# Kernel optimization log

Measured on AMD Instinct MI355X. Metric: run time of the kernel, lower is better.

The kernel has to match this reference:

```python
import jax, jax.numpy as jnp
import numpy as np

ODE_UNFOLDS = 6   # ncps LTCCell default
EPS = 1e-8
BATCH = 4096

def _conv(x, w, b, stride, pad):
    y = jax.lax.conv_general_dilated(x, w, (stride, stride), [(pad, pad), (pad, pad)],
                                     dimension_numbers=('NCHW', 'OIHW', 'NCHW'))
    return y + b[None, :, None, None]

def _bn(x, g, bta, m, v):
    # eval-mode batchnorm (running stats)
    inv = g * jax.lax.rsqrt(v + 1e-5)
    return x * inv[None, :, None, None] + (bta - m * inv)[None, :, None, None]

def _maxpool2(x):
    return jax.lax.reduce_window(x, -jnp.inf, jax.lax.max, (1, 1, 2, 2), (1, 1, 2, 2), 'VALID')

def _forward(x, conv1_w, conv1_b, conv2_w, conv2_b, bn2_g, bn2_b, bn2_m, bn2_v,
             conv3_w, conv3_b, conv4_w, conv4_b, bn4_g, bn4_b, bn4_m, bn4_v,
             input_w, input_b, sensory_mu, sensory_sigma, sensory_w, sensory_erev, sensory_mask,
             mu, sigma, w, erev, mask, gleak, vleak, cm, output_w, output_b):
    h = jax.nn.relu(_conv(x, conv1_w, conv1_b, 1, 0))                                            # [B,16,26,26]
    h = jax.nn.relu(_bn(_conv(h, conv2_w, conv2_b, 2, 2), bn2_g, bn2_b, bn2_m, bn2_v))           # [B,32,14,14]
    h = jax.nn.relu(_conv(h, conv3_w, conv3_b, 2, 2))                                            # [B,64,7,7]
    h = _maxpool2(jax.nn.relu(_bn(_conv(h, conv4_w, conv4_b, 2, 2), bn4_g, bn4_b, bn4_m, bn4_v)))  # [B,128,2,2]
    seq = h.reshape(-1, 32, 16)                                                                  # [B,T=32,F=16]
    # --- LTC cell (ncps fused ODE solver) ---
    xin = seq * input_w + input_b                                                                # affine input mapping
    # sensory synapses depend only on the input -> precompute for all timesteps
    sact = jax.nn.softplus(sensory_w) * jax.nn.sigmoid((xin[..., None] - sensory_mu) * sensory_sigma) * sensory_mask  # [B,T,16,19]
    wnum_s = jnp.einsum('btsn,sn->btn', sact, sensory_erev)   # [B,T,19]
    wden_s = jnp.sum(sact, axis=2)                            # [B,T,19]
    w_pos = jax.nn.softplus(w) * mask                         # [pre=19,post=19]
    gl = jax.nn.softplus(gleak)
    cm_t = jax.nn.softplus(cm) * ODE_UNFOLDS                  # cm / (elapsed_time=1.0 / unfolds)
    def tstep(v, nd):
        wns, wds = nd
        def unfold(v2, _):
            wa = w_pos * jax.nn.sigmoid((v2[..., None] - mu) * sigma)   # [B,19,19]
            num = cm_t * v2 + gl * vleak + jnp.sum(wa * erev, axis=1) + wns
            den = cm_t + gl + jnp.sum(wa, axis=1) + wds
            return num / (den + EPS), None
        v, _ = jax.lax.scan(unfold, v, None, length=ODE_UNFOLDS)
        return v, None
    h0 = jnp.zeros((seq.shape[0], 19), seq.dtype)
    vT, _ = jax.lax.scan(tstep, h0, (jnp.swapaxes(wnum_s, 0, 1), jnp.swapaxes(wden_s, 0, 1)))
    # out[:, -1, :] == output mapping of final state; motor neurons are the first 2
    return vT[:, :2] * output_w + output_b


def setup_inputs() -> dict:
    key = jax.random.key(0)
    ks = jax.random.split(key, 16)
    rng = np.random.default_rng(0)
    u = lambda k, s, lo, hi: jax.random.uniform(k, s, jnp.float32, lo, hi)
    n = lambda k, s, sc: jax.random.normal(k, s, jnp.float32) * sc
    inp = {}
    inp['x'] = jax.random.normal(ks[0], (BATCH, 1, 28, 28), jnp.float32)
    inp['conv1_w'] = n(ks[1], (16, 1, 3, 3), 0.3); inp['conv1_b'] = jnp.zeros(16)
    inp['conv2_w'] = n(ks[2], (32, 16, 3, 3), 0.08); inp['conv2_b'] = jnp.zeros(32)
    inp['bn2_g'] = jnp.ones(32); inp['bn2_b'] = jnp.zeros(32)
    inp['bn2_m'] = jnp.zeros(32); inp['bn2_v'] = jnp.ones(32)
    inp['conv3_w'] = n(ks[3], (64, 32, 5, 5), 0.035); inp['conv3_b'] = jnp.zeros(64)
    inp['conv4_w'] = n(ks[4], (128, 64, 5, 5), 0.025); inp['conv4_b'] = jnp.zeros(128)
    inp['bn4_g'] = jnp.ones(128); inp['bn4_b'] = jnp.zeros(128)
    inp['bn4_m'] = jnp.zeros(128); inp['bn4_v'] = jnp.ones(128)
    inp['input_w'] = jnp.ones(16); inp['input_b'] = jnp.zeros(16)
    # ncps LTCCell init ranges
    inp['sensory_mu'] = u(ks[5], (16, 19), 0.3, 0.8)
    inp['sensory_sigma'] = u(ks[6], (16, 19), 3.0, 8.0)
    inp['sensory_w'] = u(ks[7], (16, 19), 0.001, 1.0)
    inp['sensory_erev'] = jnp.asarray(rng.choice([-1.0, 1.0], (16, 19)).astype(np.float32))
    inp['sensory_mask'] = jnp.asarray((rng.random((16, 19)) < 0.35).astype(np.float32))
    inp['mu'] = u(ks[8], (19, 19), 0.3, 0.8)
    inp['sigma'] = u(ks[9], (19, 19), 3.0, 8.0)
    inp['w'] = u(ks[10], (19, 19), 0.001, 1.0)
    inp['erev'] = jnp.asarray(rng.choice([-1.0, 1.0], (19, 19)).astype(np.float32))
    inp['mask'] = jnp.asarray((rng.random((19, 19)) < 0.35).astype(np.float32))
    inp['gleak'] = u(ks[11], (19,), 0.001, 1.0)
    inp['vleak'] = u(ks[12], (19,), -0.2, 0.2)
    inp['cm'] = u(ks[13], (19,), 0.4, 0.6)
    inp['output_w'] = jnp.ones(2); inp['output_b'] = jnp.zeros(2)
    return inp


def reference(x, conv1_w, conv1_b, conv2_w, conv2_b, bn2_g, bn2_b, bn2_m, bn2_v,
              conv3_w, conv3_b, conv4_w, conv4_b, bn4_g, bn4_b, bn4_m, bn4_v,
              input_w, input_b, sensory_mu, sensory_sigma, sensory_w, sensory_erev, sensory_mask,
              mu, sigma, w, erev, mask, gleak, vleak, cm, output_w, output_b):
    return _forward(x, conv1_w, conv1_b, conv2_w, conv2_b, bn2_g, bn2_b, bn2_m, bn2_v,
                    conv3_w, conv3_b, conv4_w, conv4_b, bn4_g, bn4_b, bn4_m, bn4_v,
                    input_w, input_b, sensory_mu, sensory_sigma, sensory_w, sensory_erev, sensory_mask,
                    mu, sigma, w, erev, mask, gleak, vleak, cm, output_w, output_b)
```

## Files before the change

kernel.cpp:

```cpp
#include <hip/hip_runtime.h>

#define BATCH 4096
typedef unsigned short u16_t;

#define P_SWM   0
#define P_SWME  304
#define P_WP    608
#define P_WPE   969
#define P_GL    1330
#define P_GLVL  1349
#define P_CMT   1368
#define P_SC2   1392
#define P_SH2   1424
#define P_SC4   1456
#define P_SH4   1584

#define OFF_PAR 0L
#define OFF_B2F 2048L
#define OFF_B3F 6656L
#define OFF_B4F 57856L
#define OFF_DYN 262656L

typedef __attribute__((ext_vector_type(8))) short short8;
typedef __attribute__((ext_vector_type(16))) float f32x16;
typedef __attribute__((ext_vector_type(4))) float f32x4;
#define MFMA(a, b, c) __builtin_amdgcn_mfma_f32_32x32x16_bf16(a, b, c, 0, 0, 0)
#define MFMA16(a, b, c) __builtin_amdgcn_mfma_f32_16x16x32_bf16(a, b, c, 0, 0, 0)

#define PERM_HI(w1, w0) __builtin_amdgcn_perm((w1), (w0), 0x05040100u)
#define PERM_LO(w1, w0) __builtin_amdgcn_perm((w1), (w0), 0x07060302u)

union U8 { unsigned u[4]; short8 v; };
union A4 { f32x4 v; float f[4]; };

__device__ __forceinline__ float sigmoidf_(float x) {
    return 1.0f / (1.0f + __expf(-x));
}
__device__ __forceinline__ float softplusf_(float x) { return log1pf(__expf(x)); }

__device__ __forceinline__ unsigned splitpack(float f) {
    unsigned u = __float_as_uint(f);
    float rsd = f - __uint_as_float(u & 0xFFFF0000u);
    unsigned ur = __float_as_uint(rsd);
    ur = ur + 0x7FFFu + ((ur >> 16) & 1u);
    return (u >> 16) | (ur & 0xFFFF0000u);
}
__device__ __forceinline__ u16_t bfhalf(float v, int pl) {
    unsigned u = __float_as_uint(v);
    if (pl == 0) return (u16_t)(u >> 16);
    float rsd = v - __uint_as_float(u & 0xFFFF0000u);
    unsigned ur = __float_as_uint(rsd);
    ur = ur + 0x7FFFu + ((ur >> 16) & 1u);
    return (u16_t)(ur >> 16);
}

__global__ __launch_bounds__(256) void k_prep(
    const float* __restrict__ w2, const float* __restrict__ w3, const float* __restrict__ w4,
    const float* __restrict__ sw, const float* __restrict__ serev, const float* __restrict__ smask,
    const float* __restrict__ w,  const float* __restrict__ erev,  const float* __restrict__ mask,
    const float* __restrict__ gleak, const float* __restrict__ vleak, const float* __restrict__ cm,
    const float* __restrict__ b2, const float* __restrict__ g2, const float* __restrict__ be2,
    const float* __restrict__ m2, const float* __restrict__ v2,
    const float* __restrict__ b4, const float* __restrict__ g4, const float* __restrict__ be4,
    const float* __restrict__ m4, const float* __restrict__ v4,
    float* __restrict__ ws) {
    int gid = blockIdx.x * 256 + threadIdx.x, stride = gridDim.x * 256;
    u16_t* b2f = (u16_t*)(ws + OFF_B2F);
    u16_t* b3f = (u16_t*)(ws + OFF_B3F);
    u16_t* b4f = (u16_t*)(ws + OFF_B4F);
    for (int i = gid; i < 9216; i += stride) {
        int j = i & 7, ln = (i >> 3) & 63;
        int r = i >> 9;
        int s = r % 9, pl = r / 9;
        int k = s * 16 + (ln >> 5) * 8 + j;
        int tap = k >> 4, ci = k & 15;
        int co = ln & 31;
        b2f[i] = bfhalf(w2[(co * 16 + ci) * 9 + tap], pl);
    }
    for (int i = gid; i < 102400; i += stride) {
        int j = i & 7, ln = (i >> 3) & 63;
        int t = i >> 9;
        int tap = t % 25, r = t / 25;
        int nt = r & 3, pl = r >> 2;
        int co = nt * 16 + (ln & 15);
        int ci = (ln >> 4) * 8 + j;
        b3f[i] = bfhalf(w3[(co * 32 + ci) * 25 + tap], pl);
    }
    for (int i = gid; i < 409600; i += stride) {
        int j = i & 7, ln = (i >> 3) & 63;
        int t = i >> 9;
        int ks = t % 50, r = t / 50;
        int nt = r & 7, pl = r >> 3;
        int co = nt * 16 + (ln & 15);
        int tap = ks >> 1;
        int ci = (ks & 1) * 32 + (ln >> 4) * 8 + j;
        b4f[i] = bfhalf(w4[(co * 64 + ci) * 25 + tap], pl);
    }
    if (blockIdx.x == 0) {
        float* par = ws + OFF_PAR;
        int tid = threadIdx.x;
        for (int i = tid; i < 304; i += 256) {
            float v_ = softplusf_(sw[i]) * smask[i];
            par[P_SWM + i] = v_;
            par[P_SWME + i] = v_ * serev[i];
        }
        for (int i = tid; i < 361; i += 256) {
            float v_ = softplusf_(w[i]) * mask[i];
            par[P_WP + i] = v_;
            par[P_WPE + i] = v_ * erev[i];
        }
        for (int i = tid; i < 19; i += 256) {
            float g = softplusf_(gleak[i]);
            par[P_GL + i] = g;
            par[P_GLVL + i] = g * vleak[i];
            par[P_CMT + i] = softplusf_(cm[i]) * 6.0f;
        }
        for (int i = tid; i < 32; i += 256) {
            float inv = g2[i] * __frsqrt_rn(v2[i] + 1e-5f);
            par[P_SC2 + i] = inv;
            par[P_SH2 + i] = (b2[i] - m2[i]) * inv + be2[i];
        }
        for (int i = tid; i < 128; i += 256) {
            float inv = g4[i] * __frsqrt_rn(v4[i] + 1e-5f);
            par[P_SC4 + i] = inv;
            par[P_SH4 + i] = (b4[i] - m4[i]) * inv + be4[i];
        }
    }
}

__global__ __launch_bounds__(512, 4) void k_conv12(
    const float* __restrict__ x, const float* __restrict__ w1, const float* __restrict__ b1,
    const float* __restrict__ ws, unsigned* __restrict__ h2g) {
    __shared__ float xs[784];
    __shared__ unsigned h1s[14300];
    const float* par = ws + OFF_PAR;
    int b = blockIdx.x, tid = threadIdx.x;
    {
        for (int i = tid; i < 784; i += 512) xs[i] = x[(long)b * 784 + i];
        uint4* hz = (uint4*)h1s;
        uint4 z; z.x = z.y = z.z = z.w = 0u;
        for (int i = tid; i < 3575; i += 512) hz[i] = z;
    }
    __syncthreads();
    {
        int co = tid >> 5, slot = tid & 31;
        float wr[9];
        #pragma unroll
        for (int i = 0; i < 9; i++) wr[i] = w1[co * 9 + i];
        float bb = b1[co];
        for (int k = 0; k < 22; k++) {
            int px = slot + (k << 5);
            if (px >= 676) break;
            int oh = px / 26, ow = px % 26;
            float s = bb;
            #pragma unroll
            for (int kh = 0; kh < 3; kh++)
                #pragma unroll
                for (int kw = 0; kw < 3; kw++)
                    s = fmaf(xs[(oh + kh) * 28 + ow + kw], wr[kh * 3 + kw], s);
            h1s[((oh + 2) * 29 + (ow + 2)) * 17 + co] = splitpack(fmaxf(s, 0.f));
        }
    }
    __syncthreads();
    {
        int wv = tid >> 6, lane = tid & 63;
        int mloc = lane & 31, hf = lane >> 5, half8 = hf * 8;
        const u16_t* B2 = (const u16_t*)(ws + OFF_B2F);
        const short8* pb = (const short8*)B2 + lane;
        float sc = par[P_SC2 + mloc], sh = par[P_SH2 + mloc];
        int mt = wv;
        if (mt < 7) {
            int px = mt * 32 + mloc;
            bool pxok = px < 196;
            int pxc = pxok ? px : 195;
            int oh = pxc / 14, ow = pxc % 14;
            f32x16 acc;
            #pragma unroll
            for (int i = 0; i < 16; i++) acc[i] = 0.f;
            #pragma unroll
            for (int s = 0; s < 9; s++) {
                int kh = s / 3, kw = s % 3;
                int abase = (pxok ? ((oh * 2 + kh) * 29 + (ow * 2 + kw)) * 17 : 0) + half8;
                unsigned w_[8];
                #pragma unroll
                for (int j = 0; j < 8; j++) w_[j] = h1s[abase + j];
                U8 ah, al;
                #pragma unroll
                for (int d = 0; d < 4; d++) {
                    ah.u[d] = PERM_HI(w_[2 * d + 1], w_[2 * d]);
                    al.u[d] = PERM_LO(w_[2 * d + 1], w_[2 * d]);
                }
                short8 bh = pb[s * 64];
                short8 bl = pb[(9 + s) * 64];
                acc = MFMA(ah.v, bh, acc);
                acc = MFMA(ah.v, bl, acc);
                acc = MFMA(al.v, bh, acc);
            }
            #pragma unroll
            for (int r5 = 0; r5 < 16; r5++) {
                int row = (r5 & 3) + 8 * (r5 >> 2) + 4 * hf;
                int pxw = mt * 32 + row;
                if (pxw < 196) {
                    float y = fmaxf(fmaf(acc[r5], sc, sh), 0.f);
                    h2g[(long)b * 6272 + pxw * 32 + mloc] = splitpack(y);
                }
            }
        }
    }
}

__global__ __launch_bounds__(256, 4) void k_conv34s(
    const unsigned* __restrict__ h2g, const float* __restrict__ b3g,
    const float* __restrict__ inw, const float* __restrict__ inb,
    const float* __restrict__ smu, const float* __restrict__ ssig,
    const float* __restrict__ ws,
    float* __restrict__ wn, float* __restrict__ wd) {
    __shared__ unsigned h2s[6501];
    __shared__ unsigned h3s[3250];
    const float* par = ws + OFF_PAR;
    int b = blockIdx.x, tid = threadIdx.x;
    {
        const unsigned* src = h2g + (long)b * 6272;
        for (int i = tid; i < 6272; i += 256) h2s[(i >> 5) * 33 + (i & 31)] = src[i];
        if (tid < 33) h2s[6468 + tid] = 0u;
        if (tid < 65) h3s[3185 + tid] = 0u;
    }
    __syncthreads();
    int wv = tid >> 6;
    int lane = tid & 63;
    int n16 = lane & 15, quad = lane >> 4, quad8 = quad * 8;

    {
        int px = wv * 16 + n16;
        bool pxok = px < 49;
        int pxc = pxok ? px : 48;
        int oh = pxc / 7, ow = pxc % 7;
        int oh2 = oh * 2 - 2, ow2 = ow * 2 - 2;
        A4 acc[4];
        #pragma unroll
        for (int nt = 0; nt < 4; nt++) {
            float bi = b3g[nt * 16 + n16];
            #pragma unroll
            for (int r = 0; r < 4; r++) acc[nt].f[r] = bi;
        }
        const short8* B3 = (const short8*)(const u16_t*)(ws + OFF_B3F);
        const short8* ph0 = B3 + (0 * 25) * 64 + lane;
        const short8* ph1 = B3 + (1 * 25) * 64 + lane;
        const short8* ph2 = B3 + (2 * 25) * 64 + lane;
        const short8* ph3 = B3 + (3 * 25) * 64 + lane;
        const short8* pl0 = B3 + (4 * 25) * 64 + lane;
        const short8* pl1 = B3 + (5 * 25) * 64 + lane;
        const short8* pl2 = B3 + (6 * 25) * 64 + lane;
        const short8* pl3 = B3 + (7 * 25) * 64 + lane;
        #pragma unroll
        for (int kh = 0; kh < 5; kh++) {
            int ih = oh2 + kh;
            #pragma unroll
            for (int kw = 0; kw < 5; kw++) {
                int iw = ow2 + kw;
                bool ok = pxok && ((unsigned)ih < 14u) && ((unsigned)iw < 14u);
                int rowb = ok ? (ih * 14 + iw) * 33 : 6468;
                const unsigned* ap = h2s + rowb + quad8;
                unsigned w_[8];
                #pragma unroll
                for (int j = 0; j < 8; j++) w_[j] = ap[j];
                U8 ah, al;
                #pragma unroll
                for (int d = 0; d < 4; d++) {
                    ah.u[d] = PERM_HI(w_[2 * d + 1], w_[2 * d]);
                    al.u[d] = PERM_LO(w_[2 * d + 1], w_[2 * d]);
                }
                int s = (kh * 5 + kw) * 64;
                short8 bh, bl;
                bh = ph0[s]; bl = pl0[s];
                acc[0].v = MFMA16(ah.v, bh, acc[0].v);
                acc[0].v = MFMA16(ah.v, bl, acc[0].v);
                acc[0].v = MFMA16(al.v, bh, acc[0].v);
                bh = ph1[s]; bl = pl1[s];
                acc[1].v = MFMA16(ah.v, bh, acc[1].v);
                acc[1].v = MFMA16(ah.v, bl, acc[1].v);
                acc[1].v = MFMA16(al.v, bh, acc[1].v);
                bh = ph2[s]; bl = pl2[s];
                acc[2].v = MFMA16(ah.v, bh, acc[2].v);
                acc[2].v = MFMA16(ah.v, bl, acc[2].v);
                acc[2].v = MFMA16(al.v, bh, acc[2].v);
                bh = ph3[s]; bl = pl3[s];
                acc[3].v = MFMA16(ah.v, bh, acc[3].v);
                acc[3].v = MFMA16(ah.v, bl, acc[3].v);
                acc[3].v = MFMA16(al.v, bh, acc[3].v);
            }
        }
        #pragma unroll
        for (int nt = 0; nt < 4; nt++) {
            int co = nt * 16 + n16;
            #pragma unroll
            for (int r = 0; r < 4; r++) {
                int pxw = wv * 16 + quad * 4 + r;
                if (pxw < 49)
                    h3s[pxw * 65 + co] = splitpack(fmaxf(acc[nt].f[r], 0.f));
            }
        }
    }
    __syncthreads();
    {
        int oh = n16 >> 2, ow = n16 & 3;
        int oh2 = oh * 2 - 2, ow2 = ow * 2 - 2;
        int nt0 = wv * 2, nt1 = wv * 2 + 1;
        A4 c0, c1;
        #pragma unroll
        for (int r = 0; r < 4; r++) { c0.f[r] = 0.f; c1.f[r] = 0.f; }
        const short8* B4 = (const short8*)(const u16_t*)(ws + OFF_B4F);
        const short8* ph0 = B4 + (nt0 * 50) * 64 + lane;
        const short8* ph1 = B4 + (nt1 * 50) * 64 + lane;
        const short8* pl0 = B4 + ((8 + nt0) * 50) * 64 + lane;
        const short8* pl1 = B4 + ((8 + nt1) * 50) * 64 + lane;
        #pragma unroll
        for (int kh = 0; kh < 5; kh++) {
            int ih = oh2 + kh;
            #pragma unroll
            for (int kw = 0; kw < 5; kw++) {
                int iw = ow2 + kw;
                bool ok = ((unsigned)ih < 7u) && ((unsigned)iw < 7u);
                int rowb = ok ? (ih * 7 + iw) * 65 : 3185;
                #pragma unroll
                for (int ch = 0; ch < 2; ch++) {
                    const unsigned* ap = h3s + rowb + ch * 32 + quad8;
                    unsigned w_[8];
                    #pragma unroll
                    for (int j = 0; j < 8; j++) w_[j] = ap[j];
                    U8 ah, al;
                    #pragma unroll
                    for (int d = 0; d < 4; d++) {
                        ah.u[d] = PERM_HI(w_[2 * d + 1], w_[2 * d]);
                        al.u[d] = PERM_LO(w_[2 * d + 1], w_[2 * d]);
                    }
                    int s = ((kh * 5 + kw) * 2 + ch) * 64;
                    short8 bh, bl;
                    bh = ph0[s]; bl = pl0[s];
                    c0.v = MFMA16(ah.v, bh, c0.v);
                    c0.v = MFMA16(ah.v, bl, c0.v);
                    c0.v = MFMA16(al.v, bh, c0.v);
                    bh = ph1[s]; bl = pl1[s];
                    c1.v = MFMA16(ah.v, bh, c1.v);
                    c1.v = MFMA16(ah.v, bl, c1.v);
                    c1.v = MFMA16(al.v, bh, c1.v);
                }
            }
        }
        __syncthreads();
        float* xin_s = (float*)h2s;
        #pragma unroll
        for (int t2 = 0; t2 < 2; t2++) {
            A4* cp = t2 ? &c1 : &c0;
            int co = (t2 ? nt1 : nt0) * 16 + n16;
            float sc = par[P_SC4 + co], sh = par[P_SH4 + co];
            float y[4];
            #pragma unroll
            for (int r = 0; r < 4; r++) y[r] = fmaxf(fmaf(cp->f[r], sc, sh), 0.f);
            float p0 = fmaxf(y[0], y[1]);
            float p1 = fmaxf(y[2], y[3]);
            p0 = fmaxf(p0, __shfl_xor(p0, 16));
            p1 = fmaxf(p1, __shfl_xor(p1, 16));
            if ((quad & 1) == 0) {
                int ph = quad >> 1;
                int ts = co >> 2;
                int f0 = ((co & 3) << 2) + ph * 2;
                xin_s[ts * 16 + f0] = fmaf(p0, inw[f0], inb[f0]);
                xin_s[ts * 16 + f0 + 1] = fmaf(p1, inw[f0 + 1], inb[f0 + 1]);
            }
        }
    }
    __syncthreads();
    const float* xin_s = (const float*)h2s;
    for (int idx = tid; idx < 608; idx += 256) {
        int tt = idx / 19, n = idx - tt * 19;
        float nu = 0.f, de = 0.f;
        #pragma unroll
        for (int s = 0; s < 16; s++) {
            float sg = sigmoidf_((xin_s[tt * 16 + s] - smu[s * 19 + n]) * ssig[s * 19 + n]);
            nu = fmaf(par[P_SWME + s * 19 + n], sg, nu);
            de = fmaf(par[P_SWM + s * 19 + n], sg, de);
        }
        wn[((long)b * 32 + tt) * 19 + n] = nu;
        wd[((long)b * 32 + tt) * 19 + n] = de;
    }
}

__global__ __launch_bounds__(256, 2) void k_ltc(
    const float* __restrict__ mu_g, const float* __restrict__ sg_g,
    const float* __restrict__ ws,
    const float* __restrict__ wn, const float* __restrict__ wd,
    const float* __restrict__ outw, const float* __restrict__ outb,
    float* __restrict__ out, int img0, int nimg) {
    const float* par = ws + OFF_PAR;
    int tid = threadIdx.x, wave = tid >> 6, lane = tid & 63;
    int li = lane / 19, j = lane - li * 19;
    if (li > 2) { li = 2; j = 18; }
    int il = blockIdx.x * 12 + wave * 3 + li;
    int ilc = il < nimg ? il : nimg - 1;

    const float L2E = 1.44269504f;
    float aj[19], bj[19], wpj[19], wpej[19];
    #pragma unroll
    for (int i = 0; i < 19; i++) {
        float mu = mu_g[i * 19 + j];
        float sg = sg_g[i * 19 + j];
        aj[i] = -sg * L2E;
        bj[i] = mu * sg * L2E;
        wpj[i] = par[P_WP + i * 19 + j];
        wpej[i] = par[P_WPE + i * 19 + j];
    }
    float cmt = par[P_CMT + j], gl = par[P_GL + j], glvl = par[P_GLVL + j];
    float v = 0.f;
    long base0 = (long)ilc * 608 + j;
    float wns = wn[base0], wds = wd[base0];
    for (int t = 0; t < 32; t++) {
        float wns_n = 0.f, wds_n = 0.f;
        if (t < 31) {
            long basen = base0 + (t + 1) * 19;
            wns_n = wn[basen];
            wds_n = wd[basen];
        }
        #pragma unroll 1
        for (int u = 0; u < 6; u++) {
            float n0 = 0.f, n1 = 0.f, d0 = 0.f, d1 = 0.f;
            #pragma unroll
            for (int i = 0; i < 19; i++) {
                float vi = __shfl(v, li * 19 + i, 64);
                float e = __builtin_amdgcn_exp2f(fmaf(vi, aj[i], bj[i]));
                float s = __builtin_amdgcn_rcpf(1.0f + e);
                if (i & 1) { n1 = fmaf(wpej[i], s, n1); d1 = fmaf(wpj[i], s, d1); }
                else       { n0 = fmaf(wpej[i], s, n0); d0 = fmaf(wpj[i], s, d0); }
            }
            float num = fmaf(cmt, v, glvl) + wns + (n0 + n1);
            float den = cmt + gl + wds + (d0 + d1);
            v = num * __builtin_amdgcn_rcpf(den + 1e-8f);
        }
        wns = wns_n; wds = wds_n;
    }
    if (j < 2 && il < nimg && lane < 57)
        out[(long)(img0 + il) * 2 + j] = fmaf(v, outw[j], outb[j]);
}

extern "C" void kernel_launch(void* const* d_in, const int* in_sizes, int n_in,
                              void* d_out, int out_size, void* d_ws, size_t ws_size,
                              hipStream_t stream) {
    const float* x    = (const float*)d_in[0];
    const float* w1   = (const float*)d_in[1];
    const float* b1   = (const float*)d_in[2];
    const float* w2   = (const float*)d_in[3];
    const float* b2   = (const float*)d_in[4];
    const float* g2   = (const float*)d_in[5];
    const float* be2  = (const float*)d_in[6];
    const float* m2   = (const float*)d_in[7];
    const float* v2   = (const float*)d_in[8];
    const float* w3   = (const float*)d_in[9];
    const float* b3   = (const float*)d_in[10];
    const float* w4   = (const float*)d_in[11];
    const float* b4   = (const float*)d_in[12];
    const float* g4   = (const float*)d_in[13];
    const float* be4  = (const float*)d_in[14];
    const float* m4   = (const float*)d_in[15];
    const float* v4   = (const float*)d_in[16];
    const float* inw  = (const float*)d_in[17];
    const float* inb  = (const float*)d_in[18];
    const float* smu  = (const float*)d_in[19];
    const float* ssig = (const float*)d_in[20];
    const float* sw   = (const float*)d_in[21];
    const float* serv = (const float*)d_in[22];
    const float* smk  = (const float*)d_in[23];
    const float* mu_  = (const float*)d_in[24];
    const float* sig_ = (const float*)d_in[25];
    const float* w_   = (const float*)d_in[26];
    const float* erev = (const float*)d_in[27];
    const float* mask = (const float*)d_in[28];
    const float* glk  = (const float*)d_in[29];
    const float* vlk  = (const float*)d_in[30];
    const float* cm   = (const float*)d_in[31];
    const float* outw = (const float*)d_in[32];
    const float* outb = (const float*)d_in[33];
    float* ws = (float*)d_ws;

    k_prep<<<64, 256, 0, stream>>>(w2, w3, w4, sw, serv, smk, w_, erev, mask,
                                   glk, vlk, cm, b2, g2, be2, m2, v2,
                                   b4, g4, be4, m4, v4, ws);

    long avail = (long)(ws_size / 4) - OFF_DYN;
    long per = 6272 + 1216;
    int chunk = (int)(avail / per);
    if (chunk > BATCH) chunk = BATCH;
    if (chunk < 1) chunk = 1;

    float* wnp = ws + OFF_DYN;
    float* wdp = wnp + (long)chunk * 608;
    unsigned* h2 = (unsigned*)(wdp + (long)chunk * 608);

    for (int c0 = 0; c0 < BATCH; c0 += chunk) {
        int n = (BATCH - c0 < chunk) ? (BATCH - c0) : chunk;
        k_conv12<<<n, 512, 0, stream>>>(x + (long)c0 * 784, w1, b1, ws, h2);
        k_conv34s<<<n, 256, 0, stream>>>(h2, b3, inw, inb, smu, ssig, ws, wnp, wdp);
        k_ltc<<<(n + 11) / 12, 256, 0, stream>>>(mu_, sig_, ws, wnp, wdp, outw, outb,
                                                 (float*)d_out, c0, n);
    }
}
```

Measured before the change: 598.9 us.

## Process two images per block in conv3/conv4 to reuse weight fragments

The conv3/conv4/sensory kernel now handles two images per block. Each weight fragment loaded from global memory feeds MFMAs for both images, which halves weight-load traffic per image. In conv3 each wave takes one image and two pixel tiles. Shared memory roughly doubles and launch bounds drop from 4 to 2 blocks per CU, which lowers occupancy and raises register pressure in exchange for the weight reuse.

Measured after the change: 565.6 us. -5.6%, faster.

```diff
diff --git a/kernel.cpp b/kernel.cpp
--- a/kernel.cpp
+++ b/kernel.cpp
@@ -209,39 +209,53 @@
     }
 }
 
-__global__ __launch_bounds__(256, 4) void k_conv34s(
+__global__ __launch_bounds__(256, 2) void k_conv34s(
     const unsigned* __restrict__ h2g, const float* __restrict__ b3g,
     const float* __restrict__ inw, const float* __restrict__ inb,
     const float* __restrict__ smu, const float* __restrict__ ssig,
     const float* __restrict__ ws,
-    float* __restrict__ wn, float* __restrict__ wd) {
-    __shared__ unsigned h2s[6501];
-    __shared__ unsigned h3s[3250];
+    float* __restrict__ wn, float* __restrict__ wd, int nimg) {
+    __shared__ unsigned h2s[12969];
+    __shared__ unsigned h3s[6435];
     const float* par = ws + OFF_PAR;
     int b = blockIdx.x, tid = threadIdx.x;
+    int g0 = b * 2;
+    int g1 = (g0 + 1 < nimg) ? g0 + 1 : g0;
     {
-        const unsigned* src = h2g + (long)b * 6272;
-        for (int i = tid; i < 6272; i += 256) h2s[(i >> 5) * 33 + (i & 31)] = src[i];
-        if (tid < 33) h2s[6468 + tid] = 0u;
-        if (tid < 65) h3s[3185 + tid] = 0u;
+        const unsigned* s0 = h2g + (long)g0 * 6272;
+        const unsigned* s1 = h2g + (long)g1 * 6272;
+        for (int i = tid; i < 12544; i += 256) {
+            int img = i >= 6272;
+            int r = img ? i - 6272 : i;
+            h2s[img * 6468 + (r >> 5) * 33 + (r & 31)] = (img ? s1 : s0)[r];
+        }
+        if (tid < 33) h2s[12936 + tid] = 0u;
+        if (tid < 65) h3s[6370 + tid] = 0u;
     }
     __syncthreads();
-    int wv = tid >> 6;
-    int lane = tid & 63;
+    int wv = tid >> 6, lane = tid & 63;
     int n16 = lane & 15, quad = lane >> 4, quad8 = quad * 8;
 
     {
-        int px = wv * 16 + n16;
-        bool pxok = px < 49;
-        int pxc = pxok ? px : 48;
-        int oh = pxc / 7, ow = pxc % 7;
-        int oh2 = oh * 2 - 2, ow2 = ow * 2 - 2;
-        A4 acc[4];
+        int img = wv & 1, mhalf = wv >> 1;
+        int imgo = img * 6468;
+        int mt0 = mhalf * 2;
+        A4 acc[2][4];
         #pragma unroll
         for (int nt = 0; nt < 4; nt++) {
             float bi = b3g[nt * 16 + n16];
             #pragma unroll
-            for (int r = 0; r < 4; r++) acc[nt].f[r] = bi;
+            for (int r = 0; r < 4; r++) { acc[0][nt].f[r] = bi; acc[1][nt].f[r] = bi; }
+        }
+        int oh2[2], ow2[2];
+        bool pxok[2];
+        #pragma unroll
+        for (int mi = 0; mi < 2; mi++) {
+            int px = (mt0 + mi) * 16 + n16;
+            pxok[mi] = px < 49;
+            int pxc = pxok[mi] ? px : 48;
+            oh2[mi] = (pxc / 7) * 2 - 2;
+            ow2[mi] = (pxc % 7) * 2 - 2;
         }
         const short8* B3 = (const short8*)(const u16_t*)(ws + OFF_B3F);
         const short8* ph0 = B3 + (0 * 25) * 64 + lane;
@@ -254,77 +268,17 @@
         const short8* pl3 = B3 + (7 * 25) * 64 + lane;
         #pragma unroll
         for (int kh = 0; kh < 5; kh++) {
-            int ih = oh2 + kh;
             #pragma unroll
             for (int kw = 0; kw < 5; kw++) {
-                int iw = ow2 + kw;
-                bool ok = pxok && ((unsigned)ih < 14u) && ((unsigned)iw < 14u);
-                int rowb = ok ? (ih * 14 + iw) * 33 : 6468;
-                const unsigned* ap = h2s + rowb + quad8;
-                unsigned w_[8];
-                #pragma unroll
-                for (int j = 0; j < 8; j++) w_[j] = ap[j];
-                U8 ah, al;
-                #pragma unroll
-                for (int d = 0; d < 4; d++) {
-                    ah.u[d] = PERM_HI(w_[2 * d + 1], w_[2 * d]);
-                    al.u[d] = PERM_LO(w_[2 * d + 1], w_[2 * d]);
-                }
                 int s = (kh * 5 + kw) * 64;
-                short8 bh, bl;
-                bh = ph0[s]; bl = pl0[s];
-                acc[0].v = MFMA16(ah.v, bh, acc[0].v);
-                acc[0].v = MFMA16(ah.v, bl, acc[0].v);
-                acc[0].v = MFMA16(al.v, bh, acc[0].v);
-                bh = ph1[s]; bl = pl1[s];
-                acc[1].v = MFMA16(ah.v, bh, acc[1].v);
-                acc[1].v = MFMA16(ah.v, bl, acc[1].v);
-                acc[1].v = MFMA16(al.v, bh, acc[1].v);
-                bh = ph2[s]; bl = pl2[s];
-                acc[2].v = MFMA16(ah.v, bh, acc[2].v);
-                acc[2].v = MFMA16(ah.v, bl, acc[2].v);
-                acc[2].v = MFMA16(al.v, bh, acc[2].v);
-                bh = ph3[s]; bl = pl3[s];
-                acc[3].v = MFMA16(ah.v, bh, acc[3].v);
-                acc[3].v = MFMA16(ah.v, bl, acc[3].v);
-                acc[3].v = MFMA16(al.v, bh, acc[3].v);
-            }
-        }
-        #pragma unroll
-        for (int nt = 0; nt < 4; nt++) {
-            int co = nt * 16 + n16;
-            #pragma unroll
-            for (int r = 0; r < 4; r++) {
-                int pxw = wv * 16 + quad * 4 + r;
-                if (pxw < 49)
-                    h3s[pxw * 65 + co] = splitpack(fmaxf(acc[nt].f[r], 0.f));
-            }
-        }
-    }
-    __syncthreads();
-    {
-        int oh = n16 >> 2, ow = n16 & 3;
-        int oh2 = oh * 2 - 2, ow2 = ow * 2 - 2;
-        int nt0 = wv * 2, nt1 = wv * 2 + 1;
-        A4 c0, c1;
-        #pragma unroll
-        for (int r = 0; r < 4; r++) { c0.f[r] = 0.f; c1.f[r] = 0.f; }
-        const short8* B4 = (const short8*)(const u16_t*)(ws + OFF_B4F);
-        const short8* ph0 = B4 + (nt0 * 50) * 64 + lane;
-        const short8* ph1 = B4 + (nt1 * 50) * 64 + lane;
-        const short8* pl0 = B4 + ((8 + nt0) * 50) * 64 + lane;
-        const short8* pl1 = B4 + ((8 + nt1) * 50) * 64 + lane;
-        #pragma unroll
-        for (int kh = 0; kh < 5; kh++) {
-            int ih = oh2 + kh;
-            #pragma unroll
-            for (int kw = 0; kw < 5; kw++) {
-                int iw = ow2 + kw;
-                bool ok = ((unsigned)ih < 7u) && ((unsigned)iw < 7u);
-                int rowb = ok ? (ih * 7 + iw) * 65 : 3185;
-                #pragma unroll
-                for (int ch = 0; ch < 2; ch++) {
-                    const unsigned* ap = h3s + rowb + ch * 32 + quad8;
+                short8 bh0 = ph0[s], bh1 = ph1[s], bh2 = ph2[s], bh3 = ph3[s];
+                short8 bl0 = pl0[s], bl1 = pl1[s], bl2 = pl2[s], bl3 = pl3[s];
+                #pragma unroll
+                for (int mi = 0; mi < 2; mi++) {
+                    int ih = oh2[mi] + kh, iw = ow2[mi] + kw;
+                    bool ok = pxok[mi] && ((unsigned)ih < 14u) && ((unsigned)iw < 14u);
+                    int rowb = ok ? imgo + (ih * 14 + iw) * 33 : 12936;
+                    const unsigned* ap = h2s + rowb + quad8;
                     unsigned w_[8];
                     #pragma unroll
                     for (int j = 0; j < 8; j++) w_[j] = ap[j];
@@ -334,55 +288,127 @@
                         ah.u[d] = PERM_HI(w_[2 * d + 1], w_[2 * d]);
                         al.u[d] = PERM_LO(w_[2 * d + 1], w_[2 * d]);
                     }
+                    acc[mi][0].v = MFMA16(ah.v, bh0, acc[mi][0].v);
+                    acc[mi][0].v = MFMA16(ah.v, bl0, acc[mi][0].v);
+                    acc[mi][0].v = MFMA16(al.v, bh0, acc[mi][0].v);
+                    acc[mi][1].v = MFMA16(ah.v, bh1, acc[mi][1].v);
+                    acc[mi][1].v = MFMA16(ah.v, bl1, acc[mi][1].v);
+                    acc[mi][1].v = MFMA16(al.v, bh1, acc[mi][1].v);
+                    acc[mi][2].v = MFMA16(ah.v, bh2, acc[mi][2].v);
+                    acc[mi][2].v = MFMA16(ah.v, bl2, acc[mi][2].v);
+                    acc[mi][2].v = MFMA16(al.v, bh2, acc[mi][2].v);
+                    acc[mi][3].v = MFMA16(ah.v, bh3, acc[mi][3].v);
+                    acc[mi][3].v = MFMA16(ah.v, bl3, acc[mi][3].v);
+                    acc[mi][3].v = MFMA16(al.v, bh3, acc[mi][3].v);
+                }
+            }
+        }
+        #pragma unroll
+        for (int mi = 0; mi < 2; mi++) {
+            #pragma unroll
+            for (int nt = 0; nt < 4; nt++) {
+                int co = nt * 16 + n16;
+                #pragma unroll
+                for (int r = 0; r < 4; r++) {
+                    int pxw = (mt0 + mi) * 16 + quad * 4 + r;
+                    if (pxw < 49)
+                        h3s[img * 3185 + pxw * 65 + co] = splitpack(fmaxf(acc[mi][nt].f[r], 0.f));
+                }
+            }
+        }
+    }
+    __syncthreads();
+    {
+        int oh = n16 >> 2, ow = n16 & 3;
+        int oh2 = oh * 2 - 2, ow2 = ow * 2 - 2;
+        int nt0 = wv * 2, nt1 = nt0 + 1;
+        A4 c[2][2];
+        #pragma unroll
+        for (int mi = 0; mi < 2; mi++)
+            #pragma unroll
+            for (int r = 0; r < 4; r++) { c[mi][0].f[r] = 0.f; c[mi][1].f[r] = 0.f; }
+        const short8* B4 = (const short8*)(const u16_t*)(ws + OFF_B4F);
+        const short8* ph0 = B4 + (nt0 * 50) * 64 + lane;
+        const short8* ph1 = B4 + (nt1 * 50) * 64 + lane;
+        const short8* pl0 = B4 + ((8 + nt0) * 50) * 64 + lane;
+        const short8* pl1 = B4 + ((8 + nt1) * 50) * 64 + lane;
+        #pragma unroll
+        for (int kh = 0; kh < 5; kh++) {
+            int ih = oh2 + kh;
+            #pragma unroll
+            for (int kw = 0; kw < 5; kw++) {
+                int iw = ow2 + kw;
+                bool ok = ((unsigned)ih < 7u) && ((unsigned)iw < 7u);
+                #pragma unroll
+                for (int ch = 0; ch < 2; ch++) {
                     int s = ((kh * 5 + kw) * 2 + ch) * 64;
-                    short8 bh, bl;
-                    bh = ph0[s]; bl = pl0[s];
-                    c0.v = MFMA16(ah.v, bh, c0.v);
-                    c0.v = MFMA16(ah.v, bl, c0.v);
-                    c0.v = MFMA16(al.v, bh, c0.v);
-                    bh = ph1[s]; bl = pl1[s];
-                    c1.v = MFMA16(ah.v, bh, c1.v);
-                    c1.v = MFMA16(ah.v, bl, c1.v);
-                    c1.v = MFMA16(al.v, bh, c1.v);
+                    short8 bh0 = ph0[s], bl0 = pl0[s];
+                    short8 bh1 = ph1[s], bl1 = pl1[s];
+                    #pragma unroll
+                    for (int mi = 0; mi < 2; mi++) {
+                        int rowb = ok ? mi * 3185 + (ih * 7 + iw) * 65 + ch * 32 : 6370;
+                        const unsigned* ap = h3s + rowb + quad8;
+                        unsigned w_[8];
+                        #pragma unroll
+                        for (int j = 0; j < 8; j++) w_[j] = ap[j];
+                        U8 ah, al;
+                        #pragma unroll
+                        for (int d = 0; d < 4; d++) {
+                            ah.u[d] = PERM_HI(w_[2 * d + 1], w_[2 * d]);
+                            al.u[d] = PERM_LO(w_[2 * d + 1], w_[2 * d]);
+                        }
+                        c[mi][0].v = MFMA16(ah.v, bh0, c[mi][0].v);
+                        c[mi][0].v = MFMA16(ah.v, bl0, c[mi][0].v);
+                        c[mi][0].v = MFMA16(al.v, bh0, c[mi][0].v);
+                        c[mi][1].v = MFMA16(ah.v, bh1, c[mi][1].v);
+                        c[mi][1].v = MFMA16(ah.v, bl1, c[mi][1].v);
+                        c[mi][1].v = MFMA16(al.v, bh1, c[mi][1].v);
+                    }
                 }
             }
         }
         __syncthreads();
         float* xin_s = (float*)h2s;
         #pragma unroll
-        for (int t2 = 0; t2 < 2; t2++) {
-            A4* cp = t2 ? &c1 : &c0;
-            int co = (t2 ? nt1 : nt0) * 16 + n16;
-            float sc = par[P_SC4 + co], sh = par[P_SH4 + co];
-            float y[4];
-            #pragma unroll
-            for (int r = 0; r < 4; r++) y[r] = fmaxf(fmaf(cp->f[r], sc, sh), 0.f);
-            float p0 = fmaxf(y[0], y[1]);
-            float p1 = fmaxf(y[2], y[3]);
-            p0 = fmaxf(p0, __shfl_xor(p0, 16));
-            p1 = fmaxf(p1, __shfl_xor(p1, 16));
-            if ((quad & 1) == 0) {
-                int ph = quad >> 1;
-                int ts = co >> 2;
-                int f0 = ((co & 3) << 2) + ph * 2;
-                xin_s[ts * 16 + f0] = fmaf(p0, inw[f0], inb[f0]);
-                xin_s[ts * 16 + f0 + 1] = fmaf(p1, inw[f0 + 1], inb[f0 + 1]);
+        for (int mi = 0; mi < 2; mi++) {
+            #pragma unroll
+            for (int t2 = 0; t2 < 2; t2++) {
+                int co = (t2 ? nt1 : nt0) * 16 + n16;
+                float sc = par[P_SC4 + co], sh = par[P_SH4 + co];
+                float y[4];
+                #pragma unroll
+                for (int r = 0; r < 4; r++) y[r] = fmaxf(fmaf(c[mi][t2].f[r], sc, sh), 0.f);
+                float p0 = fmaxf(y[0], y[1]);
+                float p1 = fmaxf(y[2], y[3]);
+                p0 = fmaxf(p0, __shfl_xor(p0, 16));
+                p1 = fmaxf(p1, __shfl_xor(p1, 16));
+                if ((quad & 1) == 0) {
+                    int ph_ = quad >> 1;
+                    int ts = co >> 2;
+                    int f0 = ((co & 3) << 2) + ph_ * 2;
+                    xin_s[mi * 512 + ts * 16 + f0] = fmaf(p0, inw[f0], inb[f0]);
+                    xin_s[mi * 512 + ts * 16 + f0 + 1] = fmaf(p1, inw[f0 + 1], inb[f0 + 1]);
+                }
             }
         }
     }
     __syncthreads();
     const float* xin_s = (const float*)h2s;
-    for (int idx = tid; idx < 608; idx += 256) {
-        int tt = idx / 19, n = idx - tt * 19;
+    for (int idx = tid; idx < 1216; idx += 256) {
+        int img = idx >= 608;
+        int r = img ? idx - 608 : idx;
+        int gi = g0 + img;
+        if (gi >= nimg) break;
+        int tt = r / 19, n = r - tt * 19;
         float nu = 0.f, de = 0.f;
         #pragma unroll
         for (int s = 0; s < 16; s++) {
-            float sg = sigmoidf_((xin_s[tt * 16 + s] - smu[s * 19 + n]) * ssig[s * 19 + n]);
+            float sg = sigmoidf_((xin_s[img * 512 + tt * 16 + s] - smu[s * 19 + n]) * ssig[s * 19 + n]);
             nu = fmaf(par[P_SWME + s * 19 + n], sg, nu);
             de = fmaf(par[P_SWM + s * 19 + n], sg, de);
         }
-        wn[((long)b * 32 + tt) * 19 + n] = nu;
-        wd[((long)b * 32 + tt) * 19 + n] = de;
+        wn[((long)gi * 32 + tt) * 19 + n] = nu;
+        wd[((long)gi * 32 + tt) * 19 + n] = de;
     }
 }
 
@@ -489,7 +515,7 @@
     long per = 6272 + 1216;
     int chunk = (int)(avail / per);
     if (chunk > BATCH) chunk = BATCH;
-    if (chunk < 1) chunk = 1;
+    if (chunk < 2) chunk = 2;
 
     float* wnp = ws + OFF_DYN;
     float* wdp = wnp + (long)chunk * 608;
@@ -498,7 +524,8 @@
     for (int c0 = 0; c0 < BATCH; c0 += chunk) {
         int n = (BATCH - c0 < chunk) ? (BATCH - c0) : chunk;
         k_conv12<<<n, 512, 0, stream>>>(x + (long)c0 * 784, w1, b1, ws, h2);
-        k_conv34s<<<n, 256, 0, stream>>>(h2, b3, inw, inb, smu, ssig, ws, wnp, wdp);
+        k_conv34s<<<(n + 1) / 2, 256, 0, stream>>>(h2, b3, inw, inb, smu, ssig, ws,
+                                                   wnp, wdp, n);
         k_ltc<<<(n + 11) / 12, 256, 0, stream>>>(mu_, sig_, ws, wnp, wdp, outw, outb,
                                                  (float*)d_out, c0, n);
     }
```
